# Optimization experiments

Measured on AMD Instinct MI355X. Metric: run time of the kernel, lower is better.

The kernel has to match this reference:

```python
import jax, jax.numpy as jnp
import numpy as np

B, S, D = 2048, 8, 1280
K = 1                 # n_components_remove
HIGH_T = 0.6          # PC1_HIGH_ACTIVITY_THRESHOLD
STORM_T = 0.8         # solar_storm_threshold


def setup_inputs() -> dict:
    key = jax.random.key(0)
    k1, k2 = jax.random.split(key, 2)
    features = jax.random.normal(k1, (B, S, D), dtype=jnp.float32)
    kp_index = jax.random.uniform(k2, (B,), dtype=jnp.float32) * 9.0
    cmr_gate = jnp.ones((1,), dtype=jnp.float32)  # nn.Parameter(torch.ones(1))
    return {"features": features, "kp_index": kp_index, "cmr_gate": cmr_gate}


def reference(features, kp_index, cmr_gate):
    # Per-sample standardization over the feature axis (numpy std, ddof=0)
    mu = features.mean(axis=2, keepdims=True)            # (B, S, 1)
    sigma = features.std(axis=2, keepdims=True) + 1e-8   # (B, S, 1)
    fn = (features - mu) / sigma                         # (B, S, D)

    # Batched thin SVD of the (S, D) normalized feature matrix
    U, sv, Vt = jnp.linalg.svd(fn, full_matrices=False)  # (B,S,S), (B,S), (B,S,D)
    var = sv * sv
    pc1_ratio = var[:, 0] / (var.sum(axis=-1) + 1e-8)    # (B,)

    # solar_flag: 0 normal, 1 high activity, 2 storm
    solar_flag = (pc1_ratio >= HIGH_T).astype(jnp.int32) + (pc1_ratio >= STORM_T).astype(jnp.int32)

    # Rank-K reconstruction of the common-mode (solar) component
    low = jnp.einsum('bsk,bk,bkd->bsd', U[:, :, :K], sv[:, :K], Vt[:, :K, :])
    clean = (fn - low) * sigma + mu                      # de-normalized cleaned features

    # Kp-gating: amplify CMR when Kp >= 5
    kp_gate = 1.0 + 0.5 * (kp_index >= 5.0).astype(features.dtype)[:, None, None]
    clean = features + kp_gate * (clean - features)

    # Learnable gate
    gate = jax.nn.sigmoid(cmr_gate)[0]
    features_clean = features + gate * (clean - features)
    return features_clean, pc1_ratio, solar_flag
```

## Files before the change

### kernel.cpp

```cpp
#include <hip/hip_runtime.h>
#include <math.h>


#define SV 8
#define DV 1280
#define D4 320
#define BSTRIDE (SV*DV)

__device__ __forceinline__ float wsum(float v) {
    v += __shfl_xor(v, 32);
    v += __shfl_xor(v, 16);
    v += __shfl_xor(v, 8);
    v += __shfl_xor(v, 4);
    v += __shfl_xor(v, 2);
    v += __shfl_xor(v, 1);
    return v;
}

#define GU(i,k) ((i) <= (k) ? G[i][k] : G[k][i])
#define AU(i,k) ((i) <= (k) ? A[i][k] : A[k][i])

__global__ __launch_bounds__(64, 1)
void cmr_wave(const float* __restrict__ feat,
              const float* __restrict__ kp,
              const float* __restrict__ cmr_gate,
              float* __restrict__ out, int Bn)
{
    const int lane = threadIdx.x;
    const int b    = blockIdx.x;

    const float4* __restrict__ f4 =
        (const float4*)(feat + (size_t)b * BSTRIDE);

    float4 f[8][5];
#pragma unroll
    for (int s = 0; s < 8; ++s)
#pragma unroll
        for (int c = 0; c < 5; ++c)
            f[s][c] = f4[s * D4 + c * 64 + lane];

    float G[8][8];
    float S[8];
#pragma unroll
    for (int i = 0; i < 8; ++i) {
        S[i] = 0.f;
#pragma unroll
        for (int j = i; j < 8; ++j) G[i][j] = 0.f;
    }
#pragma unroll
    for (int c = 0; c < 5; ++c) {
#pragma unroll
        for (int i = 0; i < 8; ++i) {
            const float4 a = f[i][c];
            S[i] += (a.x + a.y) + (a.z + a.w);
#pragma unroll
            for (int j = i; j < 8; ++j) {
                const float4 q = f[j][c];
                G[i][j] = fmaf(a.x, q.x,
                          fmaf(a.y, q.y,
                          fmaf(a.z, q.z,
                          fmaf(a.w, q.w, G[i][j]))));
            }
        }
    }
#pragma unroll
    for (int i = 0; i < 8; ++i) {
        S[i] = wsum(S[i]);
#pragma unroll
        for (int j = i; j < 8; ++j) G[i][j] = wsum(G[i][j]);
    }

    float mu[8], sig[8], rsig[8];
    const float invD = 1.f / (float)DV;
#pragma unroll
    for (int i = 0; i < 8; ++i) {
        mu[i] = S[i] * invD;
        const float var = fmaxf(G[i][i] * invD - mu[i] * mu[i], 0.f);
        sig[i]  = sqrtf(var) + 1e-8f;
        rsig[i] = 1.f / sig[i];
    }
#pragma unroll
    for (int i = 0; i < 8; ++i)
#pragma unroll
        for (int j = i; j < 8; ++j)
            G[i][j] = (G[i][j] - (float)DV * mu[i] * mu[j]) * rsig[i] * rsig[j];

    float tr = 0.f;
#pragma unroll
    for (int i = 0; i < 8; ++i) tr += G[i][i];

    float A[8][8];
    {
        const float rt = 1.f / fmaxf(tr, 1e-30f);
#pragma unroll
        for (int i = 0; i < 8; ++i)
#pragma unroll
            for (int j = i; j < 8; ++j) A[i][j] = G[i][j] * rt;
    }
#pragma unroll
    for (int t = 0; t < 12; ++t) {
        float Bm[8][8];
        float trB = 0.f;
#pragma unroll
        for (int i = 0; i < 8; ++i)
#pragma unroll
            for (int j = i; j < 8; ++j) {
                float acc = 0.f;
#pragma unroll
                for (int k = 0; k < 8; ++k)
                    acc = fmaf(AU(i, k), AU(j, k), acc);
                Bm[i][j] = acc;
                if (i == j) trB += acc;
            }
        const float rt = 1.f / fmaxf(trB, 1e-30f);
#pragma unroll
        for (int i = 0; i < 8; ++i)
#pragma unroll
            for (int j = i; j < 8; ++j) A[i][j] = Bm[i][j] * rt;
    }
    int bj = 0; float best = A[0][0];
#pragma unroll
    for (int k = 1; k < 8; ++k)
        if (A[k][k] > best) { best = A[k][k]; bj = k; }
    float u[8];
#pragma unroll
    for (int i = 0; i < 8; ++i) {
        float v = AU(i, 0);
#pragma unroll
        for (int k = 1; k < 8; ++k) v = (bj == k) ? AU(i, k) : v;
        u[i] = v;
    }
    {
        float nn = 0.f;
#pragma unroll
        for (int i = 0; i < 8; ++i) nn = fmaf(u[i], u[i], nn);
        const float r = rsqrtf(fmaxf(nn, 1e-30f));
#pragma unroll
        for (int i = 0; i < 8; ++i) u[i] *= r;
    }
#pragma unroll
    for (int it = 0; it < 2; ++it) {
        float y[8]; float ny = 0.f;
#pragma unroll
        for (int i = 0; i < 8; ++i) {
            float acc = 0.f;
#pragma unroll
            for (int k = 0; k < 8; ++k) acc = fmaf(GU(i, k), u[k], acc);
            y[i] = acc; ny = fmaf(acc, acc, ny);
        }
        const float r = rsqrtf(fmaxf(ny, 1e-30f));
#pragma unroll
        for (int i = 0; i < 8; ++i) u[i] = y[i] * r;
    }
    float lam = 0.f;
#pragma unroll
    for (int i = 0; i < 8; ++i) {
        float acc = 0.f;
#pragma unroll
        for (int k = 0; k < 8; ++k) acc = fmaf(GU(i, k), u[k], acc);
        lam = fmaf(u[i], acc, lam);
    }
    const float pc1 = lam / (tr + 1e-8f);

    const float gate = 1.f / (1.f + expf(-cmr_gate[0]));
    const float kpg  = (kp[b] >= 5.0f) ? 1.5f : 1.0f;
    const float Gt   = gate * kpg;

    float av[8], cv[8];
#pragma unroll
    for (int i = 0; i < 8; ++i) {
        av[i] = u[i] * rsig[i];
        cv[i] = Gt * sig[i] * u[i];
    }
    float bc = 0.f;
#pragma unroll
    for (int i = 0; i < 8; ++i) bc = fmaf(av[i], mu[i], bc);

    if (lane == 0) {
        out[(size_t)Bn * BSTRIDE + b] = pc1;
        out[(size_t)Bn * BSTRIDE + Bn + b] =
            (pc1 >= 0.6f ? 1.f : 0.f) + (pc1 >= 0.8f ? 1.f : 0.f);
    }

    float4* __restrict__ o4 = (float4*)(out + (size_t)b * BSTRIDE);
#pragma unroll
    for (int c = 0; c < 5; ++c) {
        float4 p = make_float4(-bc, -bc, -bc, -bc);
#pragma unroll
        for (int s = 0; s < 8; ++s) {
            p.x = fmaf(av[s], f[s][c].x, p.x);
            p.y = fmaf(av[s], f[s][c].y, p.y);
            p.z = fmaf(av[s], f[s][c].z, p.z);
            p.w = fmaf(av[s], f[s][c].w, p.w);
        }
#pragma unroll
        for (int s = 0; s < 8; ++s) {
            float4 o;
            o.x = fmaf(-cv[s], p.x, f[s][c].x);
            o.y = fmaf(-cv[s], p.y, f[s][c].y);
            o.z = fmaf(-cv[s], p.z, f[s][c].z);
            o.w = fmaf(-cv[s], p.w, f[s][c].w);
            o4[s * D4 + c * 64 + lane] = o;
        }
    }
}

extern "C" void kernel_launch(void* const* d_in, const int* in_sizes, int n_in,
                              void* d_out, int out_size, void* d_ws, size_t ws_size,
                              hipStream_t stream) {
    const float* feat = (const float*)d_in[0];
    const float* kp   = (const float*)d_in[1];
    const float* gate = (const float*)d_in[2];
    float* out = (float*)d_out;
    const int Bn = in_sizes[0] / BSTRIDE;
    (void)d_ws; (void)ws_size;

    cmr_wave<<<Bn, 64, 0, stream>>>(feat, kp, gate, out, Bn);
}
```

Before: 171.6 us.

## Split each batch row across two wavefronts and re-read features instead of holding registers

Each block now uses two wavefronts that each handle half of the feature dimension with float2 loads. Partial Gram sums are combined through shared memory, and only wave 0 runs the eigen solve before broadcasting the coefficients. Features are no longer kept in registers across the solve; they are reloaded from global memory (likely hitting cache) for the output pass. This cuts register pressure and doubles the threads per row to raise occupancy and memory parallelism, at the cost of a second read, two block barriers and one wave idling during the solve.

Result: slower. 175.2 us (+2.1%).

```diff
diff --git a/kernel.cpp b/kernel.cpp
--- a/kernel.cpp
+++ b/kernel.cpp
@@ -4,8 +4,9 @@
 
 #define SV 8
 #define DV 1280
-#define D4 320
 #define BSTRIDE (SV*DV)
+#define HALF 640
+#define NCH 5
 
 __device__ __forceinline__ float wsum(float v) {
     v += __shfl_xor(v, 32);
@@ -20,24 +21,22 @@
 #define GU(i,k) ((i) <= (k) ? G[i][k] : G[k][i])
 #define AU(i,k) ((i) <= (k) ? A[i][k] : A[k][i])
 
-__global__ __launch_bounds__(64, 1)
-void cmr_wave(const float* __restrict__ feat,
+__global__ __launch_bounds__(128, 2)
+void cmr_dual(const float* __restrict__ feat,
               const float* __restrict__ kp,
               const float* __restrict__ cmr_gate,
               float* __restrict__ out, int Bn)
 {
-    const int lane = threadIdx.x;
+    __shared__ float xch[52];
+    __shared__ float cf[17];
+
+    const int tid  = threadIdx.x;
+    const int lane = tid & 63;
+    const int w    = tid >> 6;
     const int b    = blockIdx.x;
 
-    const float4* __restrict__ f4 =
-        (const float4*)(feat + (size_t)b * BSTRIDE);
-
-    float4 f[8][5];
-#pragma unroll
-    for (int s = 0; s < 8; ++s)
-#pragma unroll
-        for (int c = 0; c < 5; ++c)
-            f[s][c] = f4[s * D4 + c * 64 + lane];
+    const float* __restrict__ fb =
+        feat + (size_t)b * BSTRIDE + w * HALF + lane * 2;
 
     float G[8][8];
     float S[8];
@@ -48,19 +47,18 @@
         for (int j = i; j < 8; ++j) G[i][j] = 0.f;
     }
 #pragma unroll
-    for (int c = 0; c < 5; ++c) {
-#pragma unroll
-        for (int i = 0; i < 8; ++i) {
-            const float4 a = f[i][c];
-            S[i] += (a.x + a.y) + (a.z + a.w);
-#pragma unroll
-            for (int j = i; j < 8; ++j) {
-                const float4 q = f[j][c];
-                G[i][j] = fmaf(a.x, q.x,
-                          fmaf(a.y, q.y,
-                          fmaf(a.z, q.z,
-                          fmaf(a.w, q.w, G[i][j]))));
-            }
+    for (int c = 0; c < NCH; ++c) {
+        float2 x[8];
+#pragma unroll
+        for (int s = 0; s < 8; ++s)
+            x[s] = *(const float2*)(fb + (size_t)s * DV + c * 128);
+#pragma unroll
+        for (int i = 0; i < 8; ++i) {
+            S[i] += x[i].x + x[i].y;
+#pragma unroll
+            for (int j = i; j < 8; ++j)
+                G[i][j] = fmaf(x[i].x, x[j].x,
+                          fmaf(x[i].y, x[j].y, G[i][j]));
         }
     }
 #pragma unroll
@@ -70,137 +68,171 @@
         for (int j = i; j < 8; ++j) G[i][j] = wsum(G[i][j]);
     }
 
-    float mu[8], sig[8], rsig[8];
-    const float invD = 1.f / (float)DV;
-#pragma unroll
-    for (int i = 0; i < 8; ++i) {
-        mu[i] = S[i] * invD;
-        const float var = fmaxf(G[i][i] * invD - mu[i] * mu[i], 0.f);
-        sig[i]  = sqrtf(var) + 1e-8f;
-        rsig[i] = 1.f / sig[i];
-    }
-#pragma unroll
-    for (int i = 0; i < 8; ++i)
-#pragma unroll
-        for (int j = i; j < 8; ++j)
-            G[i][j] = (G[i][j] - (float)DV * mu[i] * mu[j]) * rsig[i] * rsig[j];
-
-    float tr = 0.f;
-#pragma unroll
-    for (int i = 0; i < 8; ++i) tr += G[i][i];
-
-    float A[8][8];
-    {
-        const float rt = 1.f / fmaxf(tr, 1e-30f);
+    if (w == 1 && lane == 0) {
+        int p = 0;
 #pragma unroll
         for (int i = 0; i < 8; ++i)
 #pragma unroll
-            for (int j = i; j < 8; ++j) A[i][j] = G[i][j] * rt;
-    }
-#pragma unroll
-    for (int t = 0; t < 12; ++t) {
-        float Bm[8][8];
-        float trB = 0.f;
+            for (int j = i; j < 8; ++j) { xch[p] = G[i][j]; ++p; }
+#pragma unroll
+        for (int i = 0; i < 8; ++i) xch[44 + i] = S[i];
+    }
+    __syncthreads();
+
+    if (w == 0) {
+        {
+            int p = 0;
+#pragma unroll
+            for (int i = 0; i < 8; ++i)
+#pragma unroll
+                for (int j = i; j < 8; ++j) { G[i][j] += xch[p]; ++p; }
+#pragma unroll
+            for (int i = 0; i < 8; ++i) S[i] += xch[44 + i];
+        }
+
+        float mu[8], sig[8], rsig[8];
+        const float invD = 1.f / (float)DV;
+#pragma unroll
+        for (int i = 0; i < 8; ++i) {
+            mu[i] = S[i] * invD;
+            const float var = fmaxf(G[i][i] * invD - mu[i] * mu[i], 0.f);
+            sig[i]  = sqrtf(var) + 1e-8f;
+            rsig[i] = 1.f / sig[i];
+        }
 #pragma unroll
         for (int i = 0; i < 8; ++i)
 #pragma unroll
-            for (int j = i; j < 8; ++j) {
+            for (int j = i; j < 8; ++j)
+                G[i][j] = (G[i][j] - (float)DV * mu[i] * mu[j]) * rsig[i] * rsig[j];
+
+        float tr = 0.f;
+#pragma unroll
+        for (int i = 0; i < 8; ++i) tr += G[i][i];
+
+        float A[8][8];
+        {
+            const float rt = 1.f / fmaxf(tr, 1e-30f);
+#pragma unroll
+            for (int i = 0; i < 8; ++i)
+#pragma unroll
+                for (int j = i; j < 8; ++j) A[i][j] = G[i][j] * rt;
+        }
+#pragma unroll
+        for (int t = 0; t < 12; ++t) {
+            float Bm[8][8];
+            float trB = 0.f;
+#pragma unroll
+            for (int i = 0; i < 8; ++i)
+#pragma unroll
+                for (int j = i; j < 8; ++j) {
+                    float acc = 0.f;
+#pragma unroll
+                    for (int k = 0; k < 8; ++k)
+                        acc = fmaf(AU(i, k), AU(j, k), acc);
+                    Bm[i][j] = acc;
+                    if (i == j) trB += acc;
+                }
+            const float rt = 1.f / fmaxf(trB, 1e-30f);
+#pragma unroll
+            for (int i = 0; i < 8; ++i)
+#pragma unroll
+                for (int j = i; j < 8; ++j) A[i][j] = Bm[i][j] * rt;
+        }
+        int bj = 0; float best = A[0][0];
+#pragma unroll
+        for (int k = 1; k < 8; ++k)
+            if (A[k][k] > best) { best = A[k][k]; bj = k; }
+        float u[8];
+#pragma unroll
+        for (int i = 0; i < 8; ++i) {
+            float v = AU(i, 0);
+#pragma unroll
+            for (int k = 1; k < 8; ++k) v = (bj == k) ? AU(i, k) : v;
+            u[i] = v;
+        }
+        {
+            float nn = 0.f;
+#pragma unroll
+            for (int i = 0; i < 8; ++i) nn = fmaf(u[i], u[i], nn);
+            const float r = rsqrtf(fmaxf(nn, 1e-30f));
+#pragma unroll
+            for (int i = 0; i < 8; ++i) u[i] *= r;
+        }
+#pragma unroll
+        for (int it = 0; it < 2; ++it) {
+            float y[8]; float ny = 0.f;
+#pragma unroll
+            for (int i = 0; i < 8; ++i) {
                 float acc = 0.f;
 #pragma unroll
-                for (int k = 0; k < 8; ++k)
-                    acc = fmaf(AU(i, k), AU(j, k), acc);
-                Bm[i][j] = acc;
-                if (i == j) trB += acc;
+                for (int k = 0; k < 8; ++k) acc = fmaf(GU(i, k), u[k], acc);
+                y[i] = acc; ny = fmaf(acc, acc, ny);
             }
-        const float rt = 1.f / fmaxf(trB, 1e-30f);
-#pragma unroll
-        for (int i = 0; i < 8; ++i)
-#pragma unroll
-            for (int j = i; j < 8; ++j) A[i][j] = Bm[i][j] * rt;
-    }
-    int bj = 0; float best = A[0][0];
-#pragma unroll
-    for (int k = 1; k < 8; ++k)
-        if (A[k][k] > best) { best = A[k][k]; bj = k; }
-    float u[8];
-#pragma unroll
-    for (int i = 0; i < 8; ++i) {
-        float v = AU(i, 0);
-#pragma unroll
-        for (int k = 1; k < 8; ++k) v = (bj == k) ? AU(i, k) : v;
-        u[i] = v;
-    }
-    {
-        float nn = 0.f;
-#pragma unroll
-        for (int i = 0; i < 8; ++i) nn = fmaf(u[i], u[i], nn);
-        const float r = rsqrtf(fmaxf(nn, 1e-30f));
-#pragma unroll
-        for (int i = 0; i < 8; ++i) u[i] *= r;
-    }
-#pragma unroll
-    for (int it = 0; it < 2; ++it) {
-        float y[8]; float ny = 0.f;
+            const float r = rsqrtf(fmaxf(ny, 1e-30f));
+#pragma unroll
+            for (int i = 0; i < 8; ++i) u[i] = y[i] * r;
+        }
+        float lam = 0.f;
 #pragma unroll
         for (int i = 0; i < 8; ++i) {
             float acc = 0.f;
 #pragma unroll
             for (int k = 0; k < 8; ++k) acc = fmaf(GU(i, k), u[k], acc);
-            y[i] = acc; ny = fmaf(acc, acc, ny);
-        }
-        const float r = rsqrtf(fmaxf(ny, 1e-30f));
-#pragma unroll
-        for (int i = 0; i < 8; ++i) u[i] = y[i] * r;
-    }
-    float lam = 0.f;
-#pragma unroll
-    for (int i = 0; i < 8; ++i) {
-        float acc = 0.f;
-#pragma unroll
-        for (int k = 0; k < 8; ++k) acc = fmaf(GU(i, k), u[k], acc);
-        lam = fmaf(u[i], acc, lam);
-    }
-    const float pc1 = lam / (tr + 1e-8f);
-
-    const float gate = 1.f / (1.f + expf(-cmr_gate[0]));
-    const float kpg  = (kp[b] >= 5.0f) ? 1.5f : 1.0f;
-    const float Gt   = gate * kpg;
+            lam = fmaf(u[i], acc, lam);
+        }
+        const float pc1 = lam / (tr + 1e-8f);
+
+        const float gate = 1.f / (1.f + expf(-cmr_gate[0]));
+        const float kpg  = (kp[b] >= 5.0f) ? 1.5f : 1.0f;
+        const float Gt   = gate * kpg;
+
+        float eav[8], ecv[8];
+#pragma unroll
+        for (int i = 0; i < 8; ++i) {
+            eav[i] = u[i] * rsig[i];
+            ecv[i] = Gt * sig[i] * u[i];
+        }
+        float ebc = 0.f;
+#pragma unroll
+        for (int i = 0; i < 8; ++i) ebc = fmaf(eav[i], mu[i], ebc);
+
+        if (lane == 0) {
+#pragma unroll
+            for (int i = 0; i < 8; ++i) { cf[i] = eav[i]; cf[8 + i] = ecv[i]; }
+            cf[16] = ebc;
+            out[(size_t)Bn * BSTRIDE + b] = pc1;
+            out[(size_t)Bn * BSTRIDE + Bn + b] =
+                (pc1 >= 0.6f ? 1.f : 0.f) + (pc1 >= 0.8f ? 1.f : 0.f);
+        }
+    }
+    __syncthreads();
 
     float av[8], cv[8];
 #pragma unroll
-    for (int i = 0; i < 8; ++i) {
-        av[i] = u[i] * rsig[i];
-        cv[i] = Gt * sig[i] * u[i];
-    }
-    float bc = 0.f;
-#pragma unroll
-    for (int i = 0; i < 8; ++i) bc = fmaf(av[i], mu[i], bc);
-
-    if (lane == 0) {
-        out[(size_t)Bn * BSTRIDE + b] = pc1;
-        out[(size_t)Bn * BSTRIDE + Bn + b] =
-            (pc1 >= 0.6f ? 1.f : 0.f) + (pc1 >= 0.8f ? 1.f : 0.f);
-    }
-
-    float4* __restrict__ o4 = (float4*)(out + (size_t)b * BSTRIDE);
-#pragma unroll
-    for (int c = 0; c < 5; ++c) {
-        float4 p = make_float4(-bc, -bc, -bc, -bc);
+    for (int s = 0; s < 8; ++s) { av[s] = cf[s]; cv[s] = cf[8 + s]; }
+    const float bc = cf[16];
+
+    float* __restrict__ ob = out + (size_t)b * BSTRIDE + w * HALF + lane * 2;
+
+#pragma unroll
+    for (int c = 0; c < NCH; ++c) {
+        float2 x[8];
+#pragma unroll
+        for (int s = 0; s < 8; ++s)
+            x[s] = *(const float2*)(fb + (size_t)s * DV + c * 128);
+
+        float2 p = make_float2(-bc, -bc);
 #pragma unroll
         for (int s = 0; s < 8; ++s) {
-            p.x = fmaf(av[s], f[s][c].x, p.x);
-            p.y = fmaf(av[s], f[s][c].y, p.y);
-            p.z = fmaf(av[s], f[s][c].z, p.z);
-            p.w = fmaf(av[s], f[s][c].w, p.w);
+            p.x = fmaf(av[s], x[s].x, p.x);
+            p.y = fmaf(av[s], x[s].y, p.y);
         }
 #pragma unroll
         for (int s = 0; s < 8; ++s) {
-            float4 o;
-            o.x = fmaf(-cv[s], p.x, f[s][c].x);
-            o.y = fmaf(-cv[s], p.y, f[s][c].y);
-            o.z = fmaf(-cv[s], p.z, f[s][c].z);
-            o.w = fmaf(-cv[s], p.w, f[s][c].w);
-            o4[s * D4 + c * 64 + lane] = o;
+            float2 o;
+            o.x = fmaf(-cv[s], p.x, x[s].x);
+            o.y = fmaf(-cv[s], p.y, x[s].y);
+            *(float2*)(ob + (size_t)s * DV + c * 128) = o;
         }
     }
 }
@@ -215,5 +247,5 @@
     const int Bn = in_sizes[0] / BSTRIDE;
     (void)d_ws; (void)ws_size;
 
-    cmr_wave<<<Bn, 64, 0, stream>>>(feat, kp, gate, out, Bn);
+    cmr_dual<<<Bn, 128, 0, stream>>>(feat, kp, gate, out, Bn);
 }
```
